# Optimization experiments

Measured on AMD Instinct MI355X. Metric: run time of the kernel, lower is better.

Reference implementation:

```python
import jax, jax.numpy as jnp
import numpy as np

N = 50000          # num_nodes
E = 1600000        # num directed edges
IN_C = 128         # in_channels
OUT_C = 128        # out_channels
HEADS = 8
HFD = OUT_C // HEADS  # head_feat_dim = 16
NEG_SLOPE = 0.2


def setup_inputs() -> dict:
    key = jax.random.key(0)
    k1, k2, k3, k4, k5 = jax.random.split(key, 5)
    node_feats = jax.random.normal(k1, (N, IN_C), dtype=jnp.float32)
    edge_index = jax.random.randint(k2, (2, E), 0, N, dtype=jnp.int64)
    # parameters (xavier-ish scale, kept small so exp() stays in range)
    W = jax.random.normal(k3, (OUT_C, IN_C), dtype=jnp.float32) * (1.0 / np.sqrt(IN_C))
    a_left = jax.random.normal(k4, (HFD, HEADS), dtype=jnp.float32) * 0.1
    a_right = jax.random.normal(k5, (HFD, HEADS), dtype=jnp.float32) * 0.1
    bias = jnp.zeros((OUT_C,), dtype=jnp.float32)
    return {"node_feats": node_feats, "edge_index": edge_index,
            "W": W, "a_left": a_left, "a_right": a_right, "bias": bias}


def reference(node_feats, edge_index, W, a_left, a_right, bias):
    n = node_feats.shape[0]
    # embedding: Linear without bias, then split into heads -> [n, h, c]
    emb = (node_feats @ W.T).reshape(n, HEADS, HFD)
    # per-node attention logit halves: sum_c emb[n,h,c] * a[c,h] -> [n, h]
    left = jnp.einsum('nhc,ch->nh', emb, a_left)
    right = jnp.einsum('nhc,ch->nh', emb, a_right)
    src = edge_index[0]
    dst = edge_index[1]
    # edge logit: score(src, dst) uses a_left on src, a_right on dst
    e = left[src] + right[dst]                       # [E, h]
    e = jnp.where(e >= 0, e, NEG_SLOPE * e)          # leaky relu(0.2)
    w = jnp.exp(e)                                   # [E, h] (module uses raw exp)
    denom = jax.ops.segment_sum(w, dst, num_segments=n)  # [n, h]
    attn = w / denom[dst]                            # [E, h]
    msg = emb[src] * attn[:, :, None]                # [E, h, c]
    out = jax.ops.segment_sum(msg, dst, num_segments=n)  # [n, h, c]
    # concat heads + bias
    out = out.reshape(n, HEADS * HFD) + bias
    return out
```

## Files before the change

### kernel.cpp

```cpp
#include <hip/hip_runtime.h>
#include <hip/hip_bf16.h>

#define N_NODES 50000
#define N_EDGES 1600000
#define HEADS 8
#define HFD 16
#define CH 128

#define PART 128
#define NB 391
#define BCAP 5120
#define PA_T 512
#define PA_CHUNK 3200
#define PA_PER 7
#define PA_BLOCKS 500

typedef __bf16 bf16x8 __attribute__((ext_vector_type(8)));
typedef __bf16 bf16x4 __attribute__((ext_vector_type(4)));
typedef float f32x4 __attribute__((ext_vector_type(4)));

__device__ __forceinline__ float bf_lo(unsigned u) { return __uint_as_float(u << 16); }
__device__ __forceinline__ float bf_hi(unsigned u) { return __uint_as_float(u & 0xffff0000u); }

__global__ __launch_bounds__(256) void k_splitw(const float* __restrict__ x,
                                                __bf16* __restrict__ hi,
                                                __bf16* __restrict__ lo,
                                                int n4,
                                                int* __restrict__ bucket_cnt) {
  int t = blockIdx.x * 256 + threadIdx.x;
  if (t < NB) bucket_cnt[t] = 0;
  if (t >= n4) return;
  f32x4 v = ((const f32x4*)x)[t];
  bf16x4 h, l;
#pragma unroll
  for (int i = 0; i < 4; ++i) {
    __bf16 hb = (__bf16)v[i];
    h[i] = hb;
    l[i] = (__bf16)(v[i] - (float)hb);
  }
  ((bf16x4*)hi)[t] = h;
  ((bf16x4*)lo)[t] = l;
}

__global__ __launch_bounds__(64) void k_emb(const float* __restrict__ X,
                                            const __bf16* __restrict__ Whi,
                                            const __bf16* __restrict__ Wlo,
                                            const float* __restrict__ aL,
                                            const float* __restrict__ aR,
                                            __bf16* __restrict__ embb,
                                            float* __restrict__ leftp,
                                            float* __restrict__ rightp) {
  int ntile = blockIdx.x;
  int lane = threadIdx.x;
  int c = lane & 15, quad = lane >> 4;
  const float* xp = X + (size_t)(ntile * 16 + c) * CH + quad * 8;
  bf16x8 xh[4], xl[4];
#pragma unroll
  for (int ks = 0; ks < 4; ++ks) {
    float4 x0 = *(const float4*)(xp + ks * 32);
    float4 x1 = *(const float4*)(xp + ks * 32 + 4);
    float xv[8] = {x0.x, x0.y, x0.z, x0.w, x1.x, x1.y, x1.z, x1.w};
#pragma unroll
    for (int j = 0; j < 8; ++j) {
      __bf16 hb = (__bf16)xv[j];
      xh[ks][j] = hb;
      xl[ks][j] = (__bf16)(xv[j] - (float)hb);
    }
  }
#pragma unroll
  for (int h = 0; h < HEADS; ++h) {
    const __bf16* wp = Whi + (size_t)(h * 16 + c) * CH + quad * 8;
    const __bf16* wlp = Wlo + (size_t)(h * 16 + c) * CH + quad * 8;
    f32x4 acc = {0.f, 0.f, 0.f, 0.f};
#pragma unroll
    for (int ks = 0; ks < 4; ++ks) {
      bf16x8 wh = *(const bf16x8*)(wp + ks * 32);
      bf16x8 wl = *(const bf16x8*)(wlp + ks * 32);
      acc = __builtin_amdgcn_mfma_f32_16x16x32_bf16(xl[ks], wh, acc, 0, 0, 0);
      acc = __builtin_amdgcn_mfma_f32_16x16x32_bf16(xh[ks], wl, acc, 0, 0, 0);
      acc = __builtin_amdgcn_mfma_f32_16x16x32_bf16(xh[ks], wh, acc, 0, 0, 0);
    }
    float aLv = aL[c * HEADS + h];
    float aRv = aR[c * HEADS + h];
#pragma unroll
    for (int r = 0; r < 4; ++r) {
      int node = ntile * 16 + quad * 4 + r;
      float v = acc[r];
      embb[(size_t)node * CH + h * HFD + c] = (__bf16)v;
      float sl = v * aLv, sr = v * aRv;
#pragma unroll
      for (int mm = 1; mm < 16; mm <<= 1) {
        sl += __shfl_xor(sl, mm);
        sr += __shfl_xor(sr, mm);
      }
      if (c == 0) {
        leftp[node * HEADS + h] = sl;
        rightp[node * HEADS + h] = sr;
      }
    }
  }
}

__global__ __launch_bounds__(PA_T) void k_bucket(const int* __restrict__ ei,
                                                 int* __restrict__ bucket_cnt,
                                                 unsigned* __restrict__ ebuf) {
  __shared__ unsigned sp[PA_CHUNK];
  __shared__ int hist[NB];
  __shared__ int lcur[NB];
  __shared__ int wbase[NB];
  __shared__ int scn[PA_T];
  int t = threadIdx.x;
  int base = blockIdx.x * PA_CHUNK;
  for (int i = t; i < NB; i += PA_T) hist[i] = 0;
  __syncthreads();
  unsigned pk[PA_PER];
#pragma unroll
  for (int i = 0; i < PA_PER; ++i) {
    int e = t + i * PA_T;
    pk[i] = 0xffffffffu;
    if (e < PA_CHUNK) {
      int src = ei[base + e];
      int dst = ei[N_EDGES + base + e];
      pk[i] = ((unsigned)(dst >> 7) << 23) | ((unsigned)(dst & 127) << 16) |
              (unsigned)src;
      atomicAdd(&hist[dst >> 7], 1);
    }
  }
  __syncthreads();
  scn[t] = (t < NB) ? hist[t] : 0;
  __syncthreads();
  int val = scn[t];
  for (int d = 1; d < PA_T; d <<= 1) {
    int o = (t >= d) ? scn[t - d] : 0;
    __syncthreads();
    val += o;
    scn[t] = val;
    __syncthreads();
  }
  if (t < NB) {
    int hv = hist[t];
    int lstart = val - hv;
    lcur[t] = lstart;
    int prior = hv ? atomicAdd(&bucket_cnt[t], hv) : 0;
    wbase[t] = t * BCAP + prior - lstart;
  }
  __syncthreads();
#pragma unroll
  for (int i = 0; i < PA_PER; ++i) {
    if (pk[i] != 0xffffffffu) {
      int b = pk[i] >> 23;
      int pos = atomicAdd(&lcur[b], 1);
      sp[pos] = pk[i];
    }
  }
  __syncthreads();
  for (int i = t; i < PA_CHUNK; i += PA_T) {
    unsigned p = sp[i];
    int b = p >> 23;
    int slot = wbase[b] + i;
    if (slot < (b + 1) * BCAP) ebuf[slot] = p;
  }
}

__global__ __launch_bounds__(512) void k_aggr(const int* __restrict__ bucket_cnt,
                                              const unsigned* __restrict__ ebuf,
                                              const __bf16* __restrict__ embb,
                                              const float* __restrict__ leftp,
                                              const float* __restrict__ rightp,
                                              const float* __restrict__ bias,
                                              float* __restrict__ out) {
  __shared__ unsigned sp[BCAP];
  __shared__ unsigned short su[BCAP];
  __shared__ int hist[PART];
  __shared__ int pfx[PART];
  __shared__ int cur[PART];
  int b = blockIdx.x >> 1;
  int half = blockIdx.x & 1;
  int t = threadIdx.x;
  int cnt = bucket_cnt[b];
  if (cnt > BCAP) cnt = BCAP;
  int ebase = b * BCAP;
  if (t < PART) hist[t] = 0;
  __syncthreads();
  for (int e = t; e < cnt; e += 512) {
    unsigned p = ebuf[ebase + e];
    sp[e] = p;
    atomicAdd(&hist[(p >> 16) & 127], 1);
  }
  __syncthreads();
  if (t < PART) pfx[t] = hist[t];
  __syncthreads();
  for (int d = 1; d < PART; d <<= 1) {
    int v = 0;
    if (t < PART) { v = pfx[t]; if (t >= d) v += pfx[t - d]; }
    __syncthreads();
    if (t < PART) pfx[t] = v;
    __syncthreads();
  }
  if (t < PART) {
    int excl = pfx[t] - hist[t];
    pfx[t] = excl;
    cur[t] = excl;
  }
  __syncthreads();
  for (int e = t; e < cnt; e += 512) {
    unsigned p = sp[e];
    int pos = atomicAdd(&cur[(p >> 16) & 127], 1);
    su[pos] = (unsigned short)(p & 0xffffu);
  }
  __syncthreads();

  int wv = t >> 6;
  int lane = t & 63;
  int g = lane >> 4;
  int m = lane & 15;
  int h = m >> 1;
#pragma unroll
  for (int k = 0; k < 8; ++k) {
    int dl = half * 64 + wv * 8 + k;
    int dst = b * PART + dl;
    bool valid = dst < N_NODES;
    int beg = pfx[dl];
    int cd = hist[dl];
    float r = valid ? rightp[dst * HEADS + h] : 0.f;
    float acc[8] = {0.f, 0.f, 0.f, 0.f, 0.f, 0.f, 0.f, 0.f};
    float dsum = 0.f;
    for (int e0 = 0; e0 < cd; e0 += 8) {
      int i0 = e0 + g, i1 = e0 + 4 + g;
      bool a0 = i0 < cd, a1 = i1 < cd;
      int s0 = su[beg + (a0 ? i0 : 0)];
      int s1 = su[beg + (a1 ? i1 : 0)];
      uint4 u0 = ((const uint4*)(embb + (size_t)s0 * CH))[m];
      uint4 u1 = ((const uint4*)(embb + (size_t)s1 * CH))[m];
      float l0 = leftp[s0 * HEADS + h];
      float l1 = leftp[s1 * HEADS + h];
      float x0 = l0 + r;
      x0 = (x0 >= 0.f) ? x0 : 0.2f * x0;
      float w0 = a0 ? __expf(x0) : 0.f;
      float x1 = l1 + r;
      x1 = (x1 >= 0.f) ? x1 : 0.2f * x1;
      float w1 = a1 ? __expf(x1) : 0.f;
      dsum += w0 + w1;
      acc[0] += w0 * bf_lo(u0.x) + w1 * bf_lo(u1.x);
      acc[1] += w0 * bf_hi(u0.x) + w1 * bf_hi(u1.x);
      acc[2] += w0 * bf_lo(u0.y) + w1 * bf_lo(u1.y);
      acc[3] += w0 * bf_hi(u0.y) + w1 * bf_hi(u1.y);
      acc[4] += w0 * bf_lo(u0.z) + w1 * bf_lo(u1.z);
      acc[5] += w0 * bf_hi(u0.z) + w1 * bf_hi(u1.z);
      acc[6] += w0 * bf_lo(u0.w) + w1 * bf_lo(u1.w);
      acc[7] += w0 * bf_hi(u0.w) + w1 * bf_hi(u1.w);
    }
#pragma unroll
    for (int mask = 16; mask <= 32; mask <<= 1) {
      dsum += __shfl_xor(dsum, mask);
#pragma unroll
      for (int j = 0; j < 8; ++j) acc[j] += __shfl_xor(acc[j], mask);
    }
    if (g == 0 && valid) {
      float inv = (dsum > 0.f) ? 1.0f / dsum : 0.f;
      float4 b0 = ((const float4*)bias)[2 * m];
      float4 b1 = ((const float4*)bias)[2 * m + 1];
      float4 o0 = {acc[0] * inv + b0.x, acc[1] * inv + b0.y,
                   acc[2] * inv + b0.z, acc[3] * inv + b0.w};
      float4 o1 = {acc[4] * inv + b1.x, acc[5] * inv + b1.y,
                   acc[6] * inv + b1.z, acc[7] * inv + b1.w};
      ((float4*)(out + (size_t)dst * CH))[2 * m] = o0;
      ((float4*)(out + (size_t)dst * CH))[2 * m + 1] = o1;
    }
  }
}

extern "C" void kernel_launch(void* const* d_in, const int* in_sizes, int n_in,
                              void* d_out, int out_size, void* d_ws, size_t ws_size,
                              hipStream_t stream) {
  const float* X = (const float*)d_in[0];
  const int* ei = (const int*)d_in[1];
  const float* W = (const float*)d_in[2];
  const float* al = (const float*)d_in[3];
  const float* ar = (const float*)d_in[4];
  const float* bias = (const float*)d_in[5];
  float* out = (float*)d_out;

  unsigned* ebuf = (unsigned*)d_ws;
  __bf16* embb = (__bf16*)(ebuf + (size_t)NB * BCAP);
  __bf16* Whi = embb + (size_t)N_NODES * CH;
  __bf16* Wlo = Whi + CH * CH;
  float* leftp = (float*)(Wlo + CH * CH);
  float* rightp = leftp + (size_t)N_NODES * HEADS;
  int* bucket_cnt = (int*)(rightp + (size_t)N_NODES * HEADS);

  k_splitw<<<(CH * CH / 4 + 255) / 256, 256, 0, stream>>>(W, Whi, Wlo, CH * CH / 4,
                                                          bucket_cnt);
  k_bucket<<<PA_BLOCKS, PA_T, 0, stream>>>(ei, bucket_cnt, ebuf);
  k_emb<<<N_NODES / 16, 64, 0, stream>>>(X, Whi, Wlo, al, ar, embb, leftp, rightp);
  k_aggr<<<NB * 2, 512, 0, stream>>>(bucket_cnt, ebuf, embb, leftp, rightp, bias, out);
}
```

Measured before the change: 215.0 us.

## Fold attention vectors into weights and compute logits via extra MFMA

```diff
diff --git a/kernel.cpp b/kernel.cpp
--- a/kernel.cpp
+++ b/kernel.cpp
@@ -22,31 +22,47 @@
 __device__ __forceinline__ float bf_lo(unsigned u) { return __uint_as_float(u << 16); }
 __device__ __forceinline__ float bf_hi(unsigned u) { return __uint_as_float(u & 0xffff0000u); }
 
-__global__ __launch_bounds__(256) void k_splitw(const float* __restrict__ x,
-                                                __bf16* __restrict__ hi,
-                                                __bf16* __restrict__ lo,
-                                                int n4,
+__global__ __launch_bounds__(256) void k_splitw(const float* __restrict__ W,
+                                                const float* __restrict__ aL,
+                                                const float* __restrict__ aR,
+                                                __bf16* __restrict__ Whi,
+                                                __bf16* __restrict__ Wlo,
+                                                __bf16* __restrict__ Vhi,
+                                                __bf16* __restrict__ Vlo,
                                                 int* __restrict__ bucket_cnt) {
   int t = blockIdx.x * 256 + threadIdx.x;
   if (t < NB) bucket_cnt[t] = 0;
-  if (t >= n4) return;
-  f32x4 v = ((const f32x4*)x)[t];
-  bf16x4 h, l;
-#pragma unroll
-  for (int i = 0; i < 4; ++i) {
-    __bf16 hb = (__bf16)v[i];
-    h[i] = hb;
-    l[i] = (__bf16)(v[i] - (float)hb);
-  }
-  ((bf16x4*)hi)[t] = h;
-  ((bf16x4*)lo)[t] = l;
+  if (t < CH * CH / 4) {
+    f32x4 v = ((const f32x4*)W)[t];
+    bf16x4 h, l;
+#pragma unroll
+    for (int i = 0; i < 4; ++i) {
+      __bf16 hb = (__bf16)v[i];
+      h[i] = hb;
+      l[i] = (__bf16)(v[i] - (float)hb);
+    }
+    ((bf16x4*)Whi)[t] = h;
+    ((bf16x4*)Wlo)[t] = l;
+  }
+  if (t < 16 * CH) {
+    int j = t >> 7;
+    int k = t & 127;
+    int h = j & 7;
+    const float* a = (j < 8) ? aL : aR;
+    float v = 0.f;
+#pragma unroll
+    for (int c = 0; c < HFD; ++c) v += W[(h * HFD + c) * CH + k] * a[c * HEADS + h];
+    __bf16 hb = (__bf16)v;
+    Vhi[t] = hb;
+    Vlo[t] = (__bf16)(v - (float)hb);
+  }
 }
 
 __global__ __launch_bounds__(64) void k_emb(const float* __restrict__ X,
                                             const __bf16* __restrict__ Whi,
                                             const __bf16* __restrict__ Wlo,
-                                            const float* __restrict__ aL,
-                                            const float* __restrict__ aR,
+                                            const __bf16* __restrict__ Vhi,
+                                            const __bf16* __restrict__ Vlo,
                                             __bf16* __restrict__ embb,
                                             float* __restrict__ leftp,
                                             float* __restrict__ rightp) {
@@ -80,23 +96,29 @@
       acc = __builtin_amdgcn_mfma_f32_16x16x32_bf16(xh[ks], wl, acc, 0, 0, 0);
       acc = __builtin_amdgcn_mfma_f32_16x16x32_bf16(xh[ks], wh, acc, 0, 0, 0);
     }
-    float aLv = aL[c * HEADS + h];
-    float aRv = aR[c * HEADS + h];
 #pragma unroll
     for (int r = 0; r < 4; ++r) {
       int node = ntile * 16 + quad * 4 + r;
-      float v = acc[r];
-      embb[(size_t)node * CH + h * HFD + c] = (__bf16)v;
-      float sl = v * aLv, sr = v * aRv;
-#pragma unroll
-      for (int mm = 1; mm < 16; mm <<= 1) {
-        sl += __shfl_xor(sl, mm);
-        sr += __shfl_xor(sr, mm);
-      }
-      if (c == 0) {
-        leftp[node * HEADS + h] = sl;
-        rightp[node * HEADS + h] = sr;
-      }
+      embb[(size_t)node * CH + h * HFD + c] = (__bf16)acc[r];
+    }
+  }
+  {
+    const __bf16* vp = Vhi + (size_t)c * CH + quad * 8;
+    const __bf16* vlp = Vlo + (size_t)c * CH + quad * 8;
+    f32x4 acc = {0.f, 0.f, 0.f, 0.f};
+#pragma unroll
+    for (int ks = 0; ks < 4; ++ks) {
+      bf16x8 vh = *(const bf16x8*)(vp + ks * 32);
+      bf16x8 vl = *(const bf16x8*)(vlp + ks * 32);
+      acc = __builtin_amdgcn_mfma_f32_16x16x32_bf16(xl[ks], vh, acc, 0, 0, 0);
+      acc = __builtin_amdgcn_mfma_f32_16x16x32_bf16(xh[ks], vl, acc, 0, 0, 0);
+      acc = __builtin_amdgcn_mfma_f32_16x16x32_bf16(xh[ks], vh, acc, 0, 0, 0);
+    }
+#pragma unroll
+    for (int r = 0; r < 4; ++r) {
+      int node = ntile * 16 + quad * 4 + r;
+      if (c < 8) leftp[node * HEADS + c] = acc[r];
+      else rightp[node * HEADS + (c - 8)] = acc[r];
     }
   }
 }
@@ -169,7 +191,6 @@
                                               const float* __restrict__ rightp,
                                               const float* __restrict__ bias,
                                               float* __restrict__ out) {
-  __shared__ unsigned sp[BCAP];
   __shared__ unsigned short su[BCAP];
   __shared__ int hist[PART];
   __shared__ int pfx[PART];
@@ -182,11 +203,8 @@
   int ebase = b * BCAP;
   if (t < PART) hist[t] = 0;
   __syncthreads();
-  for (int e = t; e < cnt; e += 512) {
-    unsigned p = ebuf[ebase + e];
-    sp[e] = p;
-    atomicAdd(&hist[(p >> 16) & 127], 1);
-  }
+  for (int e = t; e < cnt; e += 512)
+    atomicAdd(&hist[(ebuf[ebase + e] >> 16) & 127], 1);
   __syncthreads();
   if (t < PART) pfx[t] = hist[t];
   __syncthreads();
@@ -204,7 +222,7 @@
   }
   __syncthreads();
   for (int e = t; e < cnt; e += 512) {
-    unsigned p = sp[e];
+    unsigned p = ebuf[ebase + e];
     int pos = atomicAdd(&cur[(p >> 16) & 127], 1);
     su[pos] = (unsigned short)(p & 0xffffu);
   }
@@ -285,13 +303,14 @@
   __bf16* embb = (__bf16*)(ebuf + (size_t)NB * BCAP);
   __bf16* Whi = embb + (size_t)N_NODES * CH;
   __bf16* Wlo = Whi + CH * CH;
-  float* leftp = (float*)(Wlo + CH * CH);
+  __bf16* Vhi = Wlo + CH * CH;
+  __bf16* Vlo = Vhi + 16 * CH;
+  float* leftp = (float*)(Vlo + 16 * CH);
   float* rightp = leftp + (size_t)N_NODES * HEADS;
   int* bucket_cnt = (int*)(rightp + (size_t)N_NODES * HEADS);
 
-  k_splitw<<<(CH * CH / 4 + 255) / 256, 256, 0, stream>>>(W, Whi, Wlo, CH * CH / 4,
-                                                          bucket_cnt);
+  k_splitw<<<16, 256, 0, stream>>>(W, al, ar, Whi, Wlo, Vhi, Vlo, bucket_cnt);
   k_bucket<<<PA_BLOCKS, PA_T, 0, stream>>>(ei, bucket_cnt, ebuf);
-  k_emb<<<N_NODES / 16, 64, 0, stream>>>(X, Whi, Wlo, al, ar, embb, leftp, rightp);
+  k_emb<<<N_NODES / 16, 64, 0, stream>>>(X, Whi, Wlo, Vhi, Vlo, embb, leftp, rightp);
   k_aggr<<<NB * 2, 512, 0, stream>>>(bucket_cnt, ebuf, embb, leftp, rightp, bias, out);
 }
```

Measured after the change: 211.4 us. No clear change (-1.7%).
